# Kernel optimization log

Measured on AMD Instinct MI355X. Metric: run time of the kernel, lower is better.

## Reference

```python
import jax, jax.numpy as jnp
import numpy as np

NEG_SLOPE = 0.2

def _gat_attn(inp, W, a_src, a_dst):
    # inp: [G, N, C]; W: [H, C]; a_src/a_dst: [H, 1]
    x = jnp.einsum('gnc,hc->gnh', inp, W)          # Linear (no bias)
    x = jnp.where(x >= 0, x, NEG_SLOPE * x)         # LeakyReLU(0.2)
    s = jnp.einsum('gnh,ho->gn', x, a_src)          # [G, N]
    d = jnp.einsum('gnh,ho->gn', x, a_dst)          # [G, N]
    e = s[:, :, None] + d[:, None, :]               # e[g,i,j] = s_i + d_j
    return jax.nn.softmax(e, axis=-1)               # [G, N, N]

def setup_inputs() -> dict:
    key = jax.random.key(0)
    ks = jax.random.split(key, 9)
    B, C, T, J, H = 4096, 128, 10, 22, 128
    return {
        'src':     jax.random.normal(ks[0], (B, C, T, J), dtype=jnp.float32),
        'W_s':     jax.random.normal(ks[1], (H, C), dtype=jnp.float32) * 0.1,
        'a_src_s': jax.random.normal(ks[2], (H, 1), dtype=jnp.float32) * 0.1,
        'a_dst_s': jax.random.normal(ks[3], (H, 1), dtype=jnp.float32) * 0.1,
        'W_t':     jax.random.normal(ks[4], (H, C), dtype=jnp.float32) * 0.1,
        'a_src_t': jax.random.normal(ks[5], (H, 1), dtype=jnp.float32) * 0.1,
        'a_dst_t': jax.random.normal(ks[6], (H, 1), dtype=jnp.float32) * 0.1,
        'sa_bias': jax.random.normal(ks[7], (1, J, J), dtype=jnp.float32) * 0.1,
        'ta_bias': jax.random.normal(ks[8], (1, T, T), dtype=jnp.float32) * 0.1,
    }

def reference(src, W_s, a_src_s, a_dst_s, W_t, a_src_t, a_dst_t, sa_bias, ta_bias):
    B, C, T, J = src.shape
    # spatial branch: [B*T, J, C]
    sp = jnp.transpose(src, (0, 2, 3, 1)).reshape(B * T, J, C)
    sa = _gat_attn(sp, W_s, a_src_s, a_dst_s)                 # [B*T, J, J]
    # temporal branch: [B*J, T, C]
    tp = jnp.transpose(src, (0, 3, 2, 1)).reshape(B * J, T, C)
    ta = _gat_attn(tp, W_t, a_src_t, a_dst_t)                 # [B*J, T, T]
    sa_fusion = sa.reshape(B, T, J, J) + sa_bias[None]        # broadcast bias
    ta_fusion = ta.reshape(B, J, T, T) + ta_bias[None]
    zero = jnp.float32(0.0)
    return (sa_fusion, ta_fusion, zero, zero, zero, zero)
```

## Files before the change

kernel.cpp:

```cpp
#include <hip/hip_runtime.h>
#include <math.h>

#define NB 4096
#define CC 128
#define TT 10
#define JJ 22
#define MM 220
#define WSTRIDE 68
#define OUT0_N 19824640
#define OUT1_N 9011200

typedef __attribute__((ext_vector_type(8))) short bf16x8;
typedef __attribute__((ext_vector_type(4))) float f32x4;

__device__ __forceinline__ unsigned f2bf(float f) {
  union { float f; unsigned u; } v; v.f = f;
  return (v.u + 0x7FFFu + ((v.u >> 16) & 1u)) >> 16;
}

__global__ __launch_bounds__(448, 4) void dms_fused(
    const float* __restrict__ src,
    const float* __restrict__ Ws,
    const float* __restrict__ a_dst_s,
    const float* __restrict__ Wt,
    const float* __restrict__ a_dst_t,
    const float* __restrict__ sa_bias,
    const float* __restrict__ ta_bias,
    float* __restrict__ out)
{
  __shared__ unsigned lds_w[256 * WSTRIDE];
  __shared__ float a_l[256];
  __shared__ float ds_l[MM];
  __shared__ float dt_l[MM];

  const int tid  = threadIdx.x;
  const int w    = tid >> 6;
  const int lane = tid & 63;
  const int l15  = lane & 15;
  const int quad = lane >> 4;
  const int b    = blockIdx.x;

  const float* srcb = src + (size_t)b * (CC * MM);

  bf16x8 Aa[2][4];
  #pragma unroll
  for (int mtp = 0; mtp < 2; ++mtp) {
    int m = (w * 2 + mtp) * 16 + l15;
    if (m > MM - 1) m = MM - 1;
    #pragma unroll
    for (int kf = 0; kf < 4; ++kf) {
      const float* p = srcb + (kf * 32 + quad * 8) * MM + m;
      bf16x8 f;
      #pragma unroll
      for (int j = 0; j < 8; ++j)
        f[j] = (short)f2bf(p[j * MM]);
      Aa[mtp][kf] = f;
    }
  }

  for (int p4 = tid; p4 < 256 * 64; p4 += 448) {
    int n = p4 >> 6, kw = p4 & 63;
    const float* wp = (n < 128) ? (Ws + n * CC + kw * 2)
                                : (Wt + (n - 128) * CC + kw * 2);
    lds_w[n * WSTRIDE + kw] = f2bf(wp[0]) | (f2bf(wp[1]) << 16);
  }
  if (tid < 256)
    a_l[tid] = (tid < 128) ? a_dst_s[tid] : a_dst_t[tid - 128];
  __syncthreads();

  f32x4 part_s0 = {0,0,0,0}, part_s1 = {0,0,0,0};
  f32x4 part_t0 = {0,0,0,0}, part_t1 = {0,0,0,0};
  const unsigned short* wl = (const unsigned short*)lds_w;
  #pragma unroll
  for (int nt = 0; nt < 16; ++nt) {
    const bf16x8* bp = (const bf16x8*)(wl + (nt * 16 + l15) * (WSTRIDE * 2) + quad * 8);
    f32x4 acc0 = {0,0,0,0}, acc1 = {0,0,0,0};
    #pragma unroll
    for (int kf = 0; kf < 4; ++kf) {
      bf16x8 bb = bp[kf * 4];
      acc0 = __builtin_amdgcn_mfma_f32_16x16x32_bf16(Aa[0][kf], bb, acc0, 0, 0, 0);
      acc1 = __builtin_amdgcn_mfma_f32_16x16x32_bf16(Aa[1][kf], bb, acc1, 0, 0, 0);
    }
    float av = a_l[nt * 16 + l15];
    #pragma unroll
    for (int r = 0; r < 4; ++r) {
      float x0 = acc0[r]; x0 = (x0 >= 0.f) ? x0 : 0.2f * x0;
      float x1 = acc1[r]; x1 = (x1 >= 0.f) ? x1 : 0.2f * x1;
      if (nt < 8) { part_s0[r] += av * x0; part_s1[r] += av * x1; }
      else        { part_t0[r] += av * x0; part_t1[r] += av * x1; }
    }
  }

  #pragma unroll
  for (int mk = 1; mk <= 8; mk <<= 1) {
    #pragma unroll
    for (int r = 0; r < 4; ++r) {
      part_s0[r] += __shfl_xor(part_s0[r], mk);
      part_s1[r] += __shfl_xor(part_s1[r], mk);
      part_t0[r] += __shfl_xor(part_t0[r], mk);
      part_t1[r] += __shfl_xor(part_t1[r], mk);
    }
  }
  if (l15 == 0) {
    #pragma unroll
    for (int r = 0; r < 4; ++r) {
      int m0 = (w * 2) * 16 + quad * 4 + r;
      if (m0 < MM) { ds_l[m0] = part_s0[r]; dt_l[m0] = part_t0[r]; }
      int m1 = (w * 2 + 1) * 16 + quad * 4 + r;
      if (m1 < MM) { ds_l[m1] = part_s1[r]; dt_l[m1] = part_t1[r]; }
    }
  }
  __syncthreads();

  for (int t = w; t < TT; t += 7) {
    float e = (lane < JJ) ? ds_l[t * JJ + lane] : -1e30f;
    float mx = e;
    #pragma unroll
    for (int mk = 1; mk < 64; mk <<= 1) mx = fmaxf(mx, __shfl_xor(mx, mk));
    float pp = (lane < JJ) ? __expf(e - mx) : 0.f;
    float ss = pp;
    #pragma unroll
    for (int mk = 1; mk < 64; mk <<= 1) ss += __shfl_xor(ss, mk);
    pp = pp / ss;
    float* o = out + (size_t)(b * TT + t) * (JJ * JJ);
    #pragma unroll
    for (int base = 0; base < 484; base += 64) {
      int oi = base + lane;
      int jdx = oi % JJ;
      float v = __shfl(pp, jdx);
      if (oi < 484) o[oi] = v + sa_bias[oi];
    }
  }

  float* out1 = out + (size_t)OUT0_N;
  for (int jdx = w; jdx < JJ; jdx += 7) {
    float e = (lane < TT) ? dt_l[lane * JJ + jdx] : -1e30f;
    float mx = e;
    #pragma unroll
    for (int mk = 1; mk < 64; mk <<= 1) mx = fmaxf(mx, __shfl_xor(mx, mk));
    float qq = (lane < TT) ? __expf(e - mx) : 0.f;
    float ss = qq;
    #pragma unroll
    for (int mk = 1; mk < 64; mk <<= 1) ss += __shfl_xor(ss, mk);
    qq = qq / ss;
    float* o = out1 + (size_t)(b * JJ + jdx) * (TT * TT);
    #pragma unroll
    for (int base = 0; base < 128; base += 64) {
      int oi = base + lane;
      int tdx = oi % TT;
      float v = __shfl(qq, tdx);
      if (oi < 100) o[oi] = v + ta_bias[oi];
    }
  }

  if (b == 0 && tid < 4) out[(size_t)OUT0_N + OUT1_N + tid] = 0.f;
}

extern "C" void kernel_launch(void* const* d_in, const int* in_sizes, int n_in,
                              void* d_out, int out_size, void* d_ws, size_t ws_size,
                              hipStream_t stream) {
  const float* src = (const float*)d_in[0];
  const float* Ws  = (const float*)d_in[1];
  const float* ads = (const float*)d_in[3];
  const float* Wt  = (const float*)d_in[4];
  const float* adt = (const float*)d_in[6];
  const float* sab = (const float*)d_in[7];
  const float* tab = (const float*)d_in[8];
  dms_fused<<<NB, 448, 0, stream>>>(src, Ws, ads, Wt, adt, sab, tab, (float*)d_out);
}
```

Before: 738.5 us.

## Pre-pack bf16 weight fragments in a prep kernel and split waves by branch

```diff
diff --git a/kernel.cpp b/kernel.cpp
--- a/kernel.cpp
+++ b/kernel.cpp
@@ -6,30 +6,44 @@
 #define TT 10
 #define JJ 22
 #define MM 220
-#define WSTRIDE 68
 #define OUT0_N 19824640
 #define OUT1_N 9011200
 
 typedef __attribute__((ext_vector_type(8))) short bf16x8;
+typedef __attribute__((ext_vector_type(8))) unsigned short u16x8;
 typedef __attribute__((ext_vector_type(4))) float f32x4;
+
+__device__ __align__(16) unsigned short g_wf[32768];
 
 __device__ __forceinline__ unsigned f2bf(float f) {
   union { float f; unsigned u; } v; v.f = f;
   return (v.u + 0x7FFFu + ((v.u >> 16) & 1u)) >> 16;
 }
 
-__global__ __launch_bounds__(448, 4) void dms_fused(
+__global__ __launch_bounds__(256) void prep_w(
+    const float* __restrict__ Ws, const float* __restrict__ Wt)
+{
+  const int id   = blockIdx.x * 256 + threadIdx.x;
+  const int lane = id & 63;
+  const int kf   = (id >> 6) & 3;
+  const int nt   = id >> 8;
+  const int n    = nt * 16 + (lane & 15);
+  const int k0   = kf * 32 + (lane >> 4) * 8;
+  const float* row = (n < 128) ? (Ws + n * CC) : (Wt + (n - 128) * CC);
+  u16x8 v;
+  #pragma unroll
+  for (int j = 0; j < 8; ++j) v[j] = (unsigned short)f2bf(row[k0 + j]);
+  *reinterpret_cast<u16x8*>(g_wf + (size_t)id * 8) = v;
+}
+
+__global__ __launch_bounds__(896, 4) void dms_main(
     const float* __restrict__ src,
-    const float* __restrict__ Ws,
     const float* __restrict__ a_dst_s,
-    const float* __restrict__ Wt,
     const float* __restrict__ a_dst_t,
     const float* __restrict__ sa_bias,
     const float* __restrict__ ta_bias,
     float* __restrict__ out)
 {
-  __shared__ unsigned lds_w[256 * WSTRIDE];
-  __shared__ float a_l[256];
   __shared__ float ds_l[MM];
   __shared__ float dt_l[MM];
 
@@ -38,6 +52,8 @@
   const int lane = tid & 63;
   const int l15  = lane & 15;
   const int quad = lane >> 4;
+  const int mg   = w >> 1;
+  const int half = w & 1;
   const int b    = blockIdx.x;
 
   const float* srcb = src + (size_t)b * (CC * MM);
@@ -45,49 +61,40 @@
   bf16x8 Aa[2][4];
   #pragma unroll
   for (int mtp = 0; mtp < 2; ++mtp) {
-    int m = (w * 2 + mtp) * 16 + l15;
+    int m = (mg * 2 + mtp) * 16 + l15;
     if (m > MM - 1) m = MM - 1;
     #pragma unroll
-    for (int kf = 0; kf < 4; ++kf) {
-      const float* p = srcb + (kf * 32 + quad * 8) * MM + m;
+    for (int kfi = 0; kfi < 4; ++kfi) {
+      const float* p = srcb + (kfi * 32 + quad * 8) * MM + m;
       bf16x8 f;
       #pragma unroll
       for (int j = 0; j < 8; ++j)
         f[j] = (short)f2bf(p[j * MM]);
-      Aa[mtp][kf] = f;
+      Aa[mtp][kfi] = f;
     }
   }
 
-  for (int p4 = tid; p4 < 256 * 64; p4 += 448) {
-    int n = p4 >> 6, kw = p4 & 63;
-    const float* wp = (n < 128) ? (Ws + n * CC + kw * 2)
-                                : (Wt + (n - 128) * CC + kw * 2);
-    lds_w[n * WSTRIDE + kw] = f2bf(wp[0]) | (f2bf(wp[1]) << 16);
-  }
-  if (tid < 256)
-    a_l[tid] = (tid < 128) ? a_dst_s[tid] : a_dst_t[tid - 128];
-  __syncthreads();
+  const bf16x8* wfv = reinterpret_cast<const bf16x8*>(g_wf);
+  const float*  ap  = half ? a_dst_t : a_dst_s;
+  const int fbase   = half * (8 * 4 * 64);
 
-  f32x4 part_s0 = {0,0,0,0}, part_s1 = {0,0,0,0};
-  f32x4 part_t0 = {0,0,0,0}, part_t1 = {0,0,0,0};
-  const unsigned short* wl = (const unsigned short*)lds_w;
+  f32x4 part0 = {0,0,0,0}, part1 = {0,0,0,0};
   #pragma unroll
-  for (int nt = 0; nt < 16; ++nt) {
-    const bf16x8* bp = (const bf16x8*)(wl + (nt * 16 + l15) * (WSTRIDE * 2) + quad * 8);
+  for (int nt8 = 0; nt8 < 8; ++nt8) {
     f32x4 acc0 = {0,0,0,0}, acc1 = {0,0,0,0};
     #pragma unroll
-    for (int kf = 0; kf < 4; ++kf) {
-      bf16x8 bb = bp[kf * 4];
-      acc0 = __builtin_amdgcn_mfma_f32_16x16x32_bf16(Aa[0][kf], bb, acc0, 0, 0, 0);
-      acc1 = __builtin_amdgcn_mfma_f32_16x16x32_bf16(Aa[1][kf], bb, acc1, 0, 0, 0);
+    for (int kfi = 0; kfi < 4; ++kfi) {
+      bf16x8 bb = wfv[fbase + (nt8 * 4 + kfi) * 64 + lane];
+      acc0 = __builtin_amdgcn_mfma_f32_16x16x32_bf16(Aa[0][kfi], bb, acc0, 0, 0, 0);
+      acc1 = __builtin_amdgcn_mfma_f32_16x16x32_bf16(Aa[1][kfi], bb, acc1, 0, 0, 0);
     }
-    float av = a_l[nt * 16 + l15];
+    float av = ap[nt8 * 16 + l15];
     #pragma unroll
     for (int r = 0; r < 4; ++r) {
       float x0 = acc0[r]; x0 = (x0 >= 0.f) ? x0 : 0.2f * x0;
       float x1 = acc1[r]; x1 = (x1 >= 0.f) ? x1 : 0.2f * x1;
-      if (nt < 8) { part_s0[r] += av * x0; part_s1[r] += av * x1; }
-      else        { part_t0[r] += av * x0; part_t1[r] += av * x1; }
+      part0[r] += av * x0;
+      part1[r] += av * x1;
     }
   }
 
@@ -95,24 +102,24 @@
   for (int mk = 1; mk <= 8; mk <<= 1) {
     #pragma unroll
     for (int r = 0; r < 4; ++r) {
-      part_s0[r] += __shfl_xor(part_s0[r], mk);
-      part_s1[r] += __shfl_xor(part_s1[r], mk);
-      part_t0[r] += __shfl_xor(part_t0[r], mk);
-      part_t1[r] += __shfl_xor(part_t1[r], mk);
+      part0[r] += __shfl_xor(part0[r], mk);
+      part1[r] += __shfl_xor(part1[r], mk);
     }
   }
+  float* dl = half ? dt_l : ds_l;
   if (l15 == 0) {
     #pragma unroll
     for (int r = 0; r < 4; ++r) {
-      int m0 = (w * 2) * 16 + quad * 4 + r;
-      if (m0 < MM) { ds_l[m0] = part_s0[r]; dt_l[m0] = part_t0[r]; }
-      int m1 = (w * 2 + 1) * 16 + quad * 4 + r;
-      if (m1 < MM) { ds_l[m1] = part_s1[r]; dt_l[m1] = part_t1[r]; }
+      int m0 = (mg * 2) * 16 + quad * 4 + r;
+      if (m0 < MM) dl[m0] = part0[r];
+      int m1 = (mg * 2 + 1) * 16 + quad * 4 + r;
+      if (m1 < MM) dl[m1] = part1[r];
     }
   }
   __syncthreads();
 
-  for (int t = w; t < TT; t += 7) {
+  if (w < TT) {
+    const int t = w;
     float e = (lane < JJ) ? ds_l[t * JJ + lane] : -1e30f;
     float mx = e;
     #pragma unroll
@@ -133,7 +140,7 @@
   }
 
   float* out1 = out + (size_t)OUT0_N;
-  for (int jdx = w; jdx < JJ; jdx += 7) {
+  for (int jdx = w; jdx < JJ; jdx += 14) {
     float e = (lane < TT) ? dt_l[lane * JJ + jdx] : -1e30f;
     float mx = e;
     #pragma unroll
@@ -166,5 +173,6 @@
   const float* adt = (const float*)d_in[6];
   const float* sab = (const float*)d_in[7];
   const float* tab = (const float*)d_in[8];
-  dms_fused<<<NB, 448, 0, stream>>>(src, Ws, ads, Wt, adt, sab, tab, (float*)d_out);
+  prep_w<<<16, 256, 0, stream>>>(Ws, Wt);
+  dms_main<<<NB, 896, 0, stream>>>(src, ads, adt, sab, tab, (float*)d_out);
 }
```

New measurement: 769.0 us. 1.04x slower.
